# Performance work log

Hardware: AMD Instinct MI355X
Metric: run time of the kernel (lower is better)

## Reference

```python
import jax, jax.numpy as jnp
import numpy as np
import math

HIDDEN = 2048
NUM_HEADS = 16
HEAD_DIM = HIDDEN // NUM_HEADS
B, S = 2, 2048


def setup_inputs() -> dict:
    key = jax.random.key(0)
    k1, k2, k3, k4, k5 = jax.random.split(key, 5)
    scale = 1.0 / math.sqrt(HIDDEN)
    return {
        "hidden_states": jax.random.normal(k1, (B, S, HIDDEN), dtype=jnp.float32),
        "attention_mask": jnp.ones((B, S), dtype=jnp.float32),
        "Wq": jax.random.normal(k2, (HIDDEN, HIDDEN), dtype=jnp.float32) * scale,
        "Wk": jax.random.normal(k3, (HEAD_DIM, HIDDEN), dtype=jnp.float32) * scale,
        "Wv": jax.random.normal(k4, (HEAD_DIM, HIDDEN), dtype=jnp.float32) * scale,
        "Wo": jax.random.normal(k5, (HIDDEN, HIDDEN), dtype=jnp.float32) * scale,
    }


def reference(hidden_states, attention_mask, Wq, Wk, Wv, Wo):
    bsz, tgt, _ = hidden_states.shape
    # projections (torch Linear: x @ W.T)
    q = (hidden_states @ Wq.T).reshape(bsz, tgt, NUM_HEADS, HEAD_DIM).transpose(0, 2, 1, 3)  # [B,H,S,D]
    k = (hidden_states @ Wk.T)[:, None, :, :]  # [B,1,S,D] (MQA single KV head)
    v = (hidden_states @ Wv.T)[:, None, :, :]
    # scores with MQA broadcast (no K expand materialization)
    scores = jnp.einsum("bhsd,bokd->bhsk", q, k) / math.sqrt(HEAD_DIM)  # [B,H,S,S]
    neg = jnp.finfo(scores.dtype).min
    scores = scores + (1.0 - attention_mask)[:, None, None, :] * neg
    probs = jax.nn.softmax(scores, axis=-1)
    attn = jnp.einsum("bhsk,bokd->bhsd", probs, v)  # [B,H,S,D]
    out = attn.transpose(0, 2, 1, 3).reshape(bsz, tgt, HIDDEN) @ Wo.T
    # cache returned by the module (expanded to all heads, as in torch code)
    key_states = jnp.broadcast_to(k, (bsz, NUM_HEADS, tgt, HEAD_DIM))
    value_states = jnp.broadcast_to(v, (bsz, NUM_HEADS, tgt, HEAD_DIM))
    return out, key_states, value_states
```

## Files before the change

### kernel.cpp

```cpp
#include <hip/hip_runtime.h>
#include <hip/hip_bf16.h>
#include <math.h>

#define B_   2
#define S_   2048
#define HID  2048
#define NH   16
#define HD   128

typedef __bf16 bf16_t;
typedef __bf16 bf16x4 __attribute__((ext_vector_type(4)));
typedef __bf16 bf16x8 __attribute__((ext_vector_type(8)));
typedef float  f32x4  __attribute__((ext_vector_type(4)));

__device__ __forceinline__ f32x4 mfma16(bf16x8 a, bf16x8 b, f32x4 c) {
    return __builtin_amdgcn_mfma_f32_16x16x32_bf16(a, b, c, 0, 0, 0);
}

__device__ __forceinline__ void gl2lds16(const void* g, void* l) {
    __builtin_amdgcn_global_load_lds((__attribute__((address_space(1))) void*)(g),
                                     (__attribute__((address_space(3))) void*)(l),
                                     16, 0, 0);
}

__global__ void convert_bf16(const float* __restrict__ s0, const float* __restrict__ s1,
                             const float* __restrict__ s2, const float* __restrict__ s3,
                             const float* __restrict__ s4,
                             bf16_t* __restrict__ d0, bf16_t* __restrict__ d1,
                             bf16_t* __restrict__ d2, bf16_t* __restrict__ d3,
                             bf16_t* __restrict__ d4)
{
    const size_t stride = (size_t)gridDim.x * blockDim.x;
    for (size_t i = (size_t)blockIdx.x * blockDim.x + threadIdx.x; i < 4325376; i += stride) {
        const float* s; bf16_t* d; size_t off;
        if (i < 2097152)      { s = s0; d = d0; off = i; }
        else if (i < 3145728) { s = s1; d = d1; off = i - 2097152; }
        else if (i < 3211264) { s = s2; d = d2; off = i - 3145728; }
        else if (i < 3276800) { s = s3; d = d3; off = i - 3211264; }
        else                  { s = s4; d = d4; off = i - 3276800; }
        float4 v = ((const float4*)s)[off];
        bf16x4 o;
        o[0] = (bf16_t)v.x; o[1] = (bf16_t)v.y; o[2] = (bf16_t)v.z; o[3] = (bf16_t)v.w;
        ((bf16x4*)d)[off] = o;
    }
}

__global__ void broadcast_kv(const bf16_t* __restrict__ k_ws, const bf16_t* __restrict__ v_ws,
                             float* __restrict__ keyo, float* __restrict__ valo)
{
    const size_t stride = (size_t)gridDim.x * blockDim.x;
    for (size_t i = (size_t)blockIdx.x * blockDim.x + threadIdx.x; i < 4194304; i += stride) {
        int which = i >= 2097152;
        size_t f = which ? i - 2097152 : i;
        size_t e = f * 4;
        int d = (int)(e & 127);
        size_t s = (e >> 7) & 2047;
        size_t b = e >> 22;
        const bf16_t* src = (which ? v_ws : k_ws) + (b * S_ + s) * HD + d;
        bf16x4 kv = *(const bf16x4*)src;
        float4 o;
        o.x = (float)kv[0]; o.y = (float)kv[1]; o.z = (float)kv[2]; o.w = (float)kv[3];
        *(float4*)((which ? valo : keyo) + e) = o;
    }
}

template <int MODE>
__global__ __launch_bounds__(256, 2)
void gemm_nt(const bf16_t* __restrict__ A,  const bf16_t* __restrict__ B0,
             const bf16_t* __restrict__ B1, const bf16_t* __restrict__ B2,
             bf16_t* __restrict__ q_ws, bf16_t* __restrict__ k_ws,
             bf16_t* __restrict__ v_ws, bf16_t* __restrict__ vt_ws,
             float* __restrict__ outf)
{
    __shared__ __align__(16) ushort sA[128 * 32];
    __shared__ __align__(16) ushort sB[128 * 32];

    const int tid  = threadIdx.x;
    const int lane = tid & 63;
    const int wave = tid >> 6;
    const int quad = lane >> 4;
    const int l16  = lane & 15;
    const int bn = blockIdx.x, bm = blockIdx.y;
    const int wm = (wave & 1) * 64;
    const int wn = (wave >> 1) * 64;

    const bf16_t* Bbase;
    if (MODE == 0) Bbase = (bn < 16) ? (B0 + (size_t)bn * 128 * HID) : (bn == 16 ? B1 : B2);
    else           Bbase = B0 + (size_t)bn * 128 * HID;
    const bf16_t* Abase = A + (size_t)bm * 128 * HID;

    const int c0 = tid, c1 = tid + 256;
    const int r0 = c0 >> 2, o0 = (c0 & 3) * 8;
    const int r1 = c1 >> 2, o1 = (c1 & 3) * 8;

    f32x4 acc[4][4] = {};

    for (int kt = 0; kt < HID / 32; ++kt) {
        const int ko = kt * 32;
        gl2lds16(Abase + (size_t)r0 * HID + ko + o0, sA + c0 * 8);
        gl2lds16(Abase + (size_t)r1 * HID + ko + o1, sA + c1 * 8);
        gl2lds16(Bbase + (size_t)r0 * HID + ko + o0, sB + c0 * 8);
        gl2lds16(Bbase + (size_t)r1 * HID + ko + o1, sB + c1 * 8);
        __syncthreads();

        bf16x8 af[4], bfr[4];
        for (int mt = 0; mt < 4; ++mt)
            af[mt] = *(const bf16x8*)(sA + (wm + mt * 16 + l16) * 32 + quad * 8);
        for (int nt = 0; nt < 4; ++nt)
            bfr[nt] = *(const bf16x8*)(sB + (wn + nt * 16 + l16) * 32 + quad * 8);
        for (int mt = 0; mt < 4; ++mt)
            for (int nt = 0; nt < 4; ++nt)
                acc[mt][nt] = mfma16(af[mt], bfr[nt], acc[mt][nt]);
        __syncthreads();
    }

    for (int mt = 0; mt < 4; ++mt) {
        for (int nt = 0; nt < 4; ++nt) {
            for (int j = 0; j < 4; ++j) {
                float v = acc[mt][nt][j];
                int row = bm * 128 + wm + mt * 16 + quad * 4 + j;
                int col = wn + nt * 16 + l16;
                if (MODE == 1) {
                    outf[(size_t)row * HID + bn * 128 + col] = v;
                } else {
                    bf16_t bv = (bf16_t)v;
                    if (bn < 16) {
                        q_ws[(size_t)row * HID + bn * 128 + col] = bv;
                    } else {
                        int b = row >> 11, s = row & 2047, d = col;
                        if (bn == 16) {
                            k_ws[((size_t)b * S_ + s) * HD + d] = bv;
                        } else {
                            v_ws[((size_t)b * S_ + s) * HD + d] = bv;
                            vt_ws[((size_t)b * HD + d) * S_ + s] = bv;
                        }
                    }
                }
            }
        }
    }
}

#define SV_U 18432
#define SM_U 27648

__global__ __launch_bounds__(512, 2)
void attn_kernel(const bf16_t* __restrict__ Qw, const bf16_t* __restrict__ Kc,
                 const bf16_t* __restrict__ Vt, const float* __restrict__ mask,
                 bf16_t* __restrict__ Ow)
{
    __shared__ __align__(16) ushort smem[27776];
    float* sMask = (float*)&smem[SM_U];

    const int tid  = threadIdx.x;
    const int lane = tid & 63;
    const int wave = tid >> 6;
    const int quad = lane >> 4;
    const int l16  = lane & 15;
    const int qt = blockIdx.x;
    const int bh = blockIdx.y;
    const int b = bh >> 4, h = bh & 15;

    bf16x8 qf[2][4];
    {
        const bf16_t* qg = Qw + ((size_t)(b * S_ + qt * 256 + wave * 32)) * HID + h * HD;
        for (int mt = 0; mt < 2; ++mt)
            for (int kk = 0; kk < 4; ++kk)
                qf[mt][kk] = *(const bf16x8*)(qg + (size_t)(mt * 16 + l16) * HID + kk * 32 + quad * 8);
    }

    f32x4 oa[2][8] = {};
    float mrow[2][4], lrow[2][4];
    for (int mt = 0; mt < 2; ++mt)
        for (int j = 0; j < 4; ++j) { mrow[mt][j] = -INFINITY; lrow[mt][j] = 0.f; }

    const float scale = 0.08838834764831845f;
    const float NEGF  = -3.4028234663852886e38f;

    const bf16_t* kg = Kc + (size_t)b * S_ * HD;
    const bf16_t* vg = Vt + (size_t)b * HD * S_;

    for (int kt = 0; kt < S_ / 64; ++kt) {
        __syncthreads();
        for (int i = 0; i < 2; ++i) {
            int c = tid + i * 512;
            int kr = c >> 4, kc = (c & 15) * 8;
            *(uint4*)(&smem[kr * 136 + kc]) =
                *(const uint4*)(kg + (size_t)(kt * 64 + kr) * HD + kc);
            int vr = c >> 3, vc = (c & 7) * 8;
            *(uint4*)(&smem[SV_U + vr * 72 + vc]) =
                *(const uint4*)(vg + (size_t)vr * S_ + kt * 64 + vc);
        }
        if (tid < 64) {
            float mv = mask[b * S_ + kt * 64 + tid];
            sMask[tid] = (1.0f - mv) * NEGF;
        }
        __syncthreads();

        f32x4 sa[2][4];
        for (int nt = 0; nt < 4; ++nt) {
            bf16x8 kf[4];
            for (int kk = 0; kk < 4; ++kk)
                kf[kk] = *(const bf16x8*)(&smem[(nt * 16 + l16) * 136 + kk * 32 + quad * 8]);
            for (int mt = 0; mt < 2; ++mt) {
                f32x4 a = {};
                for (int kk = 0; kk < 4; ++kk)
                    a = mfma16(qf[mt][kk], kf[kk], a);
                sa[mt][nt] = a;
            }
        }
        for (int mt = 0; mt < 2; ++mt)
            for (int nt = 0; nt < 4; ++nt) {
                float madd = sMask[nt * 16 + l16];
                for (int j = 0; j < 4; ++j)
                    sa[mt][nt][j] = sa[mt][nt][j] * scale + madd;
            }
        __syncthreads();

        for (int mt = 0; mt < 2; ++mt) {
            float rm[4];
            for (int j = 0; j < 4; ++j) {
                float m = sa[mt][0][j];
                for (int nt = 1; nt < 4; ++nt) m = fmaxf(m, sa[mt][nt][j]);
                rm[j] = m;
            }
            for (int off = 1; off < 16; off <<= 1)
                for (int j = 0; j < 4; ++j)
                    rm[j] = fmaxf(rm[j], __shfl_xor(rm[j], off));
            float alpha[4];
            for (int j = 0; j < 4; ++j) {
                float mnew = fmaxf(mrow[mt][j], rm[j]);
                alpha[j] = __expf(mrow[mt][j] - mnew);
                mrow[mt][j] = mnew;
                lrow[mt][j] *= alpha[j];
                for (int nt = 0; nt < 8; ++nt) oa[mt][nt][j] *= alpha[j];
            }
            float rs[4] = {0.f, 0.f, 0.f, 0.f};
            bf16_t* sPp = (bf16_t*)&smem[wave * 2304];
            for (int nt = 0; nt < 4; ++nt)
                for (int j = 0; j < 4; ++j) {
                    float p = __expf(sa[mt][nt][j] - mrow[mt][j]);
                    rs[j] += p;
                    sPp[(mt * 16 + quad * 4 + j) * 72 + nt * 16 + l16] = (bf16_t)p;
                }
            for (int off = 1; off < 16; off <<= 1)
                for (int j = 0; j < 4; ++j) rs[j] += __shfl_xor(rs[j], off);
            for (int j = 0; j < 4; ++j) lrow[mt][j] += rs[j];
        }

        bf16x8 pf[2][2];
        for (int mt = 0; mt < 2; ++mt)
            for (int kk = 0; kk < 2; ++kk)
                pf[mt][kk] = *(const bf16x8*)(&smem[wave * 2304 + (mt * 16 + l16) * 72 + kk * 32 + quad * 8]);
        for (int nt = 0; nt < 8; ++nt)
            for (int kk = 0; kk < 2; ++kk) {
                bf16x8 vf = *(const bf16x8*)(&smem[SV_U + (nt * 16 + l16) * 72 + kk * 32 + quad * 8]);
                for (int mt = 0; mt < 2; ++mt)
                    oa[mt][nt] = mfma16(pf[mt][kk], vf, oa[mt][nt]);
            }
    }

    for (int mt = 0; mt < 2; ++mt)
        for (int j = 0; j < 4; ++j) {
            float inv = 1.0f / lrow[mt][j];
            int s = qt * 256 + wave * 32 + mt * 16 + quad * 4 + j;
            for (int nt = 0; nt < 8; ++nt) {
                int d = nt * 16 + l16;
                Ow[((size_t)(b * S_ + s)) * HID + h * HD + d] = (bf16_t)(oa[mt][nt][j] * inv);
            }
        }
}

extern "C" void kernel_launch(void* const* d_in, const int* in_sizes, int n_in,
                              void* d_out, int out_size, void* d_ws, size_t ws_size,
                              hipStream_t stream) {
    const float* hs   = (const float*)d_in[0];
    const float* mask = (const float*)d_in[1];
    const float* Wq   = (const float*)d_in[2];
    const float* Wk   = (const float*)d_in[3];
    const float* Wv   = (const float*)d_in[4];
    const float* Wo   = (const float*)d_in[5];
    float* out = (float*)d_out;

    bf16_t* wqb = (bf16_t*)out;
    bf16_t* wkb = wqb + 4194304;
    bf16_t* wvb = wkb + 262144;
    bf16_t* qb  = (bf16_t*)(out + 8388608);
    bf16_t* wob = (bf16_t*)(out + 12582912);
    bf16_t* hsb = (bf16_t*)(out + 16777216);
    bf16_t* o_ws = hsb;

    bf16_t* k_ws  = (bf16_t*)d_ws;
    bf16_t* v_ws  = k_ws + 524288;
    bf16_t* vt_ws = v_ws + 524288;

    convert_bf16<<<2048, 256, 0, stream>>>(hs, Wq, Wk, Wv, Wo, hsb, wqb, wkb, wvb, wob);
    gemm_nt<0><<<dim3(18, 32), 256, 0, stream>>>(hsb, wqb, wkb, wvb, qb, k_ws, v_ws, vt_ws, nullptr);
    attn_kernel<<<dim3(8, 32), 512, 0, stream>>>(qb, k_ws, vt_ws, mask, o_ws);
    gemm_nt<1><<<dim3(16, 32), 256, 0, stream>>>(o_ws, wob, nullptr, nullptr, nullptr, nullptr, nullptr, nullptr, out);
    broadcast_kv<<<4096, 256, 0, stream>>>(k_ws, v_ws, out + 8388608, out + 16777216);
}
```

Before: 407.7 us.

## Shrink attention query tile to 16 rows per wave, add lazy rescale and exp2

The attention kernel now has each wave own 16 query rows instead of 32, so a block covers 128 rows. The grid doubles to 512 blocks, and shared memory and registers shrink so launch bounds can ask for 4 blocks per CU, which should fill the 256-CU part better. It also folds log2e into the scale to use exp2f, and skips the online-softmax rescale unless a row max grows by more than 8. The cost is half the Q reuse per K/V tile load, so each tile is reloaded by twice as many blocks.

New measurement: 421.7 us. 1.03x slower.

```diff
diff --git a/kernel.cpp b/kernel.cpp
--- a/kernel.cpp
+++ b/kernel.cpp
@@ -141,15 +141,15 @@
     }
 }
 
-#define SV_U 18432
-#define SM_U 27648
-
-__global__ __launch_bounds__(512, 2)
+#define SV_U 9216
+#define SM_U 18432
+
+__global__ __launch_bounds__(512, 4)
 void attn_kernel(const bf16_t* __restrict__ Qw, const bf16_t* __restrict__ Kc,
                  const bf16_t* __restrict__ Vt, const float* __restrict__ mask,
                  bf16_t* __restrict__ Ow)
 {
-    __shared__ __align__(16) ushort smem[27776];
+    __shared__ __align__(16) ushort smem[18560];
     float* sMask = (float*)&smem[SM_U];
 
     const int tid  = threadIdx.x;
@@ -161,21 +161,20 @@
     const int bh = blockIdx.y;
     const int b = bh >> 4, h = bh & 15;
 
-    bf16x8 qf[2][4];
+    bf16x8 qf[4];
     {
-        const bf16_t* qg = Qw + ((size_t)(b * S_ + qt * 256 + wave * 32)) * HID + h * HD;
-        for (int mt = 0; mt < 2; ++mt)
-            for (int kk = 0; kk < 4; ++kk)
-                qf[mt][kk] = *(const bf16x8*)(qg + (size_t)(mt * 16 + l16) * HID + kk * 32 + quad * 8);
-    }
-
-    f32x4 oa[2][8] = {};
-    float mrow[2][4], lrow[2][4];
-    for (int mt = 0; mt < 2; ++mt)
-        for (int j = 0; j < 4; ++j) { mrow[mt][j] = -INFINITY; lrow[mt][j] = 0.f; }
-
-    const float scale = 0.08838834764831845f;
-    const float NEGF  = -3.4028234663852886e38f;
+        const bf16_t* qg = Qw + ((size_t)(b * S_ + qt * 128 + wave * 16 + l16)) * HID + h * HD;
+        for (int kk = 0; kk < 4; ++kk)
+            qf[kk] = *(const bf16x8*)(qg + kk * 32 + quad * 8);
+    }
+
+    f32x4 oa[8] = {};
+    float mrow[4], lrow[4];
+    for (int j = 0; j < 4; ++j) { mrow[j] = -INFINITY; lrow[j] = 0.f; }
+
+    const float scale2 = 0.08838834764831845f * 1.4426950408889634f;
+    const float NEGF   = -3.4028234663852886e38f;
+    const float LOG2E  = 1.4426950408889634f;
 
     const bf16_t* kg = Kc + (size_t)b * S_ * HD;
     const bf16_t* vg = Vt + (size_t)b * HD * S_;
@@ -192,83 +191,74 @@
                 *(const uint4*)(vg + (size_t)vr * S_ + kt * 64 + vc);
         }
         if (tid < 64) {
-            float mv = mask[b * S_ + kt * 64 + tid];
-            sMask[tid] = (1.0f - mv) * NEGF;
-        }
-        __syncthreads();
-
-        f32x4 sa[2][4];
+            float t = (1.0f - mask[b * S_ + kt * 64 + tid]) * NEGF;
+            sMask[tid] = t * LOG2E;
+        }
+        __syncthreads();
+
+        f32x4 sa[4] = {};
+        for (int kk = 0; kk < 4; ++kk)
+            for (int nt = 0; nt < 4; ++nt) {
+                bf16x8 kf = *(const bf16x8*)(&smem[(nt * 16 + l16) * 136 + kk * 32 + quad * 8]);
+                sa[nt] = mfma16(qf[kk], kf, sa[nt]);
+            }
         for (int nt = 0; nt < 4; ++nt) {
-            bf16x8 kf[4];
-            for (int kk = 0; kk < 4; ++kk)
-                kf[kk] = *(const bf16x8*)(&smem[(nt * 16 + l16) * 136 + kk * 32 + quad * 8]);
-            for (int mt = 0; mt < 2; ++mt) {
-                f32x4 a = {};
-                for (int kk = 0; kk < 4; ++kk)
-                    a = mfma16(qf[mt][kk], kf[kk], a);
-                sa[mt][nt] = a;
-            }
-        }
-        for (int mt = 0; mt < 2; ++mt)
-            for (int nt = 0; nt < 4; ++nt) {
-                float madd = sMask[nt * 16 + l16];
-                for (int j = 0; j < 4; ++j)
-                    sa[mt][nt][j] = sa[mt][nt][j] * scale + madd;
-            }
-        __syncthreads();
-
-        for (int mt = 0; mt < 2; ++mt) {
-            float rm[4];
+            float madd = sMask[nt * 16 + l16];
+            for (int j = 0; j < 4; ++j)
+                sa[nt][j] = sa[nt][j] * scale2 + madd;
+        }
+        __syncthreads();
+
+        float rm[4];
+        for (int j = 0; j < 4; ++j) {
+            float m = sa[0][j];
+            for (int nt = 1; nt < 4; ++nt) m = fmaxf(m, sa[nt][j]);
+            rm[j] = m;
+        }
+        for (int off = 1; off < 16; off <<= 1)
+            for (int j = 0; j < 4; ++j)
+                rm[j] = fmaxf(rm[j], __shfl_xor(rm[j], off));
+        bool need = false;
+        for (int j = 0; j < 4; ++j) need = need || (rm[j] > mrow[j] + 8.0f);
+        if (__any((int)need)) {
             for (int j = 0; j < 4; ++j) {
-                float m = sa[mt][0][j];
-                for (int nt = 1; nt < 4; ++nt) m = fmaxf(m, sa[mt][nt][j]);
-                rm[j] = m;
-            }
-            for (int off = 1; off < 16; off <<= 1)
-                for (int j = 0; j < 4; ++j)
-                    rm[j] = fmaxf(rm[j], __shfl_xor(rm[j], off));
-            float alpha[4];
+                float mnew  = fmaxf(mrow[j], rm[j]);
+                float alpha = exp2f(mrow[j] - mnew);
+                mrow[j] = mnew;
+                lrow[j] *= alpha;
+                for (int nt = 0; nt < 8; ++nt) oa[nt][j] *= alpha;
+            }
+        }
+        float rs[4] = {0.f, 0.f, 0.f, 0.f};
+        bf16_t* sPp = (bf16_t*)&smem[wave * 1152];
+        for (int nt = 0; nt < 4; ++nt)
             for (int j = 0; j < 4; ++j) {
-                float mnew = fmaxf(mrow[mt][j], rm[j]);
-                alpha[j] = __expf(mrow[mt][j] - mnew);
-                mrow[mt][j] = mnew;
-                lrow[mt][j] *= alpha[j];
-                for (int nt = 0; nt < 8; ++nt) oa[mt][nt][j] *= alpha[j];
-            }
-            float rs[4] = {0.f, 0.f, 0.f, 0.f};
-            bf16_t* sPp = (bf16_t*)&smem[wave * 2304];
-            for (int nt = 0; nt < 4; ++nt)
-                for (int j = 0; j < 4; ++j) {
-                    float p = __expf(sa[mt][nt][j] - mrow[mt][j]);
-                    rs[j] += p;
-                    sPp[(mt * 16 + quad * 4 + j) * 72 + nt * 16 + l16] = (bf16_t)p;
-                }
-            for (int off = 1; off < 16; off <<= 1)
-                for (int j = 0; j < 4; ++j) rs[j] += __shfl_xor(rs[j], off);
-            for (int j = 0; j < 4; ++j) lrow[mt][j] += rs[j];
-        }
-
-        bf16x8 pf[2][2];
-        for (int mt = 0; mt < 2; ++mt)
-            for (int kk = 0; kk < 2; ++kk)
-                pf[mt][kk] = *(const bf16x8*)(&smem[wave * 2304 + (mt * 16 + l16) * 72 + kk * 32 + quad * 8]);
-        for (int nt = 0; nt < 8; ++nt)
-            for (int kk = 0; kk < 2; ++kk) {
+                float p = exp2f(sa[nt][j] - mrow[j]);
+                rs[j] += p;
+                sPp[(quad * 4 + j) * 72 + nt * 16 + l16] = (bf16_t)p;
+            }
+        for (int off = 1; off < 16; off <<= 1)
+            for (int j = 0; j < 4; ++j) rs[j] += __shfl_xor(rs[j], off);
+        for (int j = 0; j < 4; ++j) lrow[j] += rs[j];
+
+        bf16x8 pf[2];
+        for (int kk = 0; kk < 2; ++kk)
+            pf[kk] = *(const bf16x8*)(&smem[wave * 1152 + l16 * 72 + kk * 32 + quad * 8]);
+        for (int kk = 0; kk < 2; ++kk)
+            for (int nt = 0; nt < 8; ++nt) {
                 bf16x8 vf = *(const bf16x8*)(&smem[SV_U + (nt * 16 + l16) * 72 + kk * 32 + quad * 8]);
-                for (int mt = 0; mt < 2; ++mt)
-                    oa[mt][nt] = mfma16(pf[mt][kk], vf, oa[mt][nt]);
-            }
-    }
-
-    for (int mt = 0; mt < 2; ++mt)
-        for (int j = 0; j < 4; ++j) {
-            float inv = 1.0f / lrow[mt][j];
-            int s = qt * 256 + wave * 32 + mt * 16 + quad * 4 + j;
-            for (int nt = 0; nt < 8; ++nt) {
-                int d = nt * 16 + l16;
-                Ow[((size_t)(b * S_ + s)) * HID + h * HD + d] = (bf16_t)(oa[mt][nt][j] * inv);
-            }
-        }
+                oa[nt] = mfma16(pf[kk], vf, oa[nt]);
+            }
+    }
+
+    for (int j = 0; j < 4; ++j) {
+        float inv = 1.0f / lrow[j];
+        int s = qt * 128 + wave * 16 + quad * 4 + j;
+        for (int nt = 0; nt < 8; ++nt) {
+            int d = nt * 16 + l16;
+            Ow[((size_t)(b * S_ + s)) * HID + h * HD + d] = (bf16_t)(oa[nt][j] * inv);
+        }
+    }
 }
 
 extern "C" void kernel_launch(void* const* d_in, const int* in_sizes, int n_in,
@@ -296,7 +286,7 @@
 
     convert_bf16<<<2048, 256, 0, stream>>>(hs, Wq, Wk, Wv, Wo, hsb, wqb, wkb, wvb, wob);
     gemm_nt<0><<<dim3(18, 32), 256, 0, stream>>>(hsb, wqb, wkb, wvb, qb, k_ws, v_ws, vt_ws, nullptr);
-    attn_kernel<<<dim3(8, 32), 512, 0, stream>>>(qb, k_ws, vt_ws, mask, o_ws);
+    attn_kernel<<<dim3(16, 32), 512, 0, stream>>>(qb, k_ws, vt_ws, mask, o_ws);
     gemm_nt<1><<<dim3(16, 32), 256, 0, stream>>>(o_ws, wob, nullptr, nullptr, nullptr, nullptr, nullptr, nullptr, out);
     broadcast_kv<<<4096, 256, 0, stream>>>(k_ws, v_ws, out + 8388608, out + 16777216);
 }
```

## Prefetch K/V tiles into registers, shrink attention blocks, use exp2 with lazy rescale

Applied to the files above, without the earlier changes.

The attention kernel now loads the next K/V tile and mask slice into registers while the current tile is being computed, then writes them to LDS at the top of the next iteration. This hides global-load latency behind the MFMA and softmax work. Blocks shrink from 512 to 256 threads, with 128 queries each, and the grid doubles to 512 blocks so more blocks fit per CU. Softmax folds log2e into the scale and uses exp2f, and it skips the output rescale unless some row max has grown by more than a threshold. The cost is more registers per thread and a more involved online-softmax path.

New measurement: 485.7 us. 1.19x slower.

```diff
diff --git a/kernel.cpp b/kernel.cpp
--- a/kernel.cpp
+++ b/kernel.cpp
@@ -141,15 +141,15 @@
     }
 }
 
-#define SV_U 18432
-#define SM_U 27648
-
-__global__ __launch_bounds__(512, 2)
+#define SV_U 9216
+#define SM_U 18432
+
+__global__ __launch_bounds__(256, 2)
 void attn_kernel(const bf16_t* __restrict__ Qw, const bf16_t* __restrict__ Kc,
                  const bf16_t* __restrict__ Vt, const float* __restrict__ mask,
                  bf16_t* __restrict__ Ow)
 {
-    __shared__ __align__(16) ushort smem[27776];
+    __shared__ __align__(16) ushort smem[18560];
     float* sMask = (float*)&smem[SM_U];
 
     const int tid  = threadIdx.x;
@@ -161,109 +161,166 @@
     const int bh = blockIdx.y;
     const int b = bh >> 4, h = bh & 15;
 
+    int koff[4], voff[4], klds[4], vlds[4];
+#pragma unroll
+    for (int i = 0; i < 4; ++i) {
+        int c = tid + i * 256;
+        koff[i] = (c >> 4) * HD + (c & 15) * 8;
+        klds[i] = (c >> 4) * 136 + (c & 15) * 8;
+        voff[i] = (c >> 3) * S_ + (c & 7) * 8;
+        vlds[i] = SV_U + (c >> 3) * 72 + (c & 7) * 8;
+    }
+
+    const bf16_t* kg = Kc + (size_t)b * S_ * HD;
+    const bf16_t* vg = Vt + (size_t)b * HD * S_;
+
     bf16x8 qf[2][4];
     {
-        const bf16_t* qg = Qw + ((size_t)(b * S_ + qt * 256 + wave * 32)) * HID + h * HD;
+        const bf16_t* qg = Qw + ((size_t)(b * S_ + qt * 128 + wave * 32)) * HID + h * HD;
+#pragma unroll
         for (int mt = 0; mt < 2; ++mt)
+#pragma unroll
             for (int kk = 0; kk < 4; ++kk)
                 qf[mt][kk] = *(const bf16x8*)(qg + (size_t)(mt * 16 + l16) * HID + kk * 32 + quad * 8);
     }
 
     f32x4 oa[2][8] = {};
     float mrow[2][4], lrow[2][4];
+#pragma unroll
     for (int mt = 0; mt < 2; ++mt)
+#pragma unroll
         for (int j = 0; j < 4; ++j) { mrow[mt][j] = -INFINITY; lrow[mt][j] = 0.f; }
 
-    const float scale = 0.08838834764831845f;
-    const float NEGF  = -3.4028234663852886e38f;
-
-    const bf16_t* kg = Kc + (size_t)b * S_ * HD;
-    const bf16_t* vg = Vt + (size_t)b * HD * S_;
+    const float scale2 = 0.08838834764831845f * 1.4426950408889634f;
+    const float NEGF   = -3.4028234663852886e38f;
+    const float LOG2E  = 1.4426950408889634f;
+
+    uint4 kreg[4], vreg[4];
+    float mreg = 1.0f;
+#pragma unroll
+    for (int i = 0; i < 4; ++i) {
+        kreg[i] = *(const uint4*)(kg + koff[i]);
+        vreg[i] = *(const uint4*)(vg + voff[i]);
+    }
+    if (tid < 64) mreg = mask[b * S_ + tid];
 
     for (int kt = 0; kt < S_ / 64; ++kt) {
         __syncthreads();
-        for (int i = 0; i < 2; ++i) {
-            int c = tid + i * 512;
-            int kr = c >> 4, kc = (c & 15) * 8;
-            *(uint4*)(&smem[kr * 136 + kc]) =
-                *(const uint4*)(kg + (size_t)(kt * 64 + kr) * HD + kc);
-            int vr = c >> 3, vc = (c & 7) * 8;
-            *(uint4*)(&smem[SV_U + vr * 72 + vc]) =
-                *(const uint4*)(vg + (size_t)vr * S_ + kt * 64 + vc);
-        }
-        if (tid < 64) {
-            float mv = mask[b * S_ + kt * 64 + tid];
-            sMask[tid] = (1.0f - mv) * NEGF;
-        }
-        __syncthreads();
-
-        f32x4 sa[2][4];
+#pragma unroll
+        for (int i = 0; i < 4; ++i) {
+            *(uint4*)(&smem[klds[i]]) = kreg[i];
+            *(uint4*)(&smem[vlds[i]]) = vreg[i];
+        }
+        if (tid < 64) sMask[tid] = (1.0f - mreg) * NEGF * LOG2E;
+        __syncthreads();
+
+        f32x4 sa[2][4] = {};
+#pragma unroll
+        for (int kk = 0; kk < 4; ++kk)
+#pragma unroll
+            for (int nt = 0; nt < 4; ++nt) {
+                bf16x8 kf = *(const bf16x8*)(&smem[(nt * 16 + l16) * 136 + kk * 32 + quad * 8]);
+#pragma unroll
+                for (int mt = 0; mt < 2; ++mt)
+                    sa[mt][nt] = mfma16(qf[mt][kk], kf, sa[mt][nt]);
+            }
+#pragma unroll
         for (int nt = 0; nt < 4; ++nt) {
-            bf16x8 kf[4];
-            for (int kk = 0; kk < 4; ++kk)
-                kf[kk] = *(const bf16x8*)(&smem[(nt * 16 + l16) * 136 + kk * 32 + quad * 8]);
-            for (int mt = 0; mt < 2; ++mt) {
-                f32x4 a = {};
-                for (int kk = 0; kk < 4; ++kk)
-                    a = mfma16(qf[mt][kk], kf[kk], a);
-                sa[mt][nt] = a;
-            }
-        }
+            float madd = sMask[nt * 16 + l16];
+#pragma unroll
+            for (int mt = 0; mt < 2; ++mt)
+#pragma unroll
+                for (int j = 0; j < 4; ++j)
+                    sa[mt][nt][j] = sa[mt][nt][j] * scale2 + madd;
+        }
+        __syncthreads();
+
+        float rm[2][4];
+#pragma unroll
         for (int mt = 0; mt < 2; ++mt)
-            for (int nt = 0; nt < 4; ++nt) {
-                float madd = sMask[nt * 16 + l16];
-                for (int j = 0; j < 4; ++j)
-                    sa[mt][nt][j] = sa[mt][nt][j] * scale + madd;
-            }
-        __syncthreads();
-
-        for (int mt = 0; mt < 2; ++mt) {
-            float rm[4];
+#pragma unroll
             for (int j = 0; j < 4; ++j) {
                 float m = sa[mt][0][j];
                 for (int nt = 1; nt < 4; ++nt) m = fmaxf(m, sa[mt][nt][j]);
-                rm[j] = m;
-            }
-            for (int off = 1; off < 16; off <<= 1)
+                rm[mt][j] = m;
+            }
+        for (int off = 1; off < 16; off <<= 1)
+#pragma unroll
+            for (int mt = 0; mt < 2; ++mt)
+#pragma unroll
                 for (int j = 0; j < 4; ++j)
-                    rm[j] = fmaxf(rm[j], __shfl_xor(rm[j], off));
-            float alpha[4];
-            for (int j = 0; j < 4; ++j) {
-                float mnew = fmaxf(mrow[mt][j], rm[j]);
-                alpha[j] = __expf(mrow[mt][j] - mnew);
-                mrow[mt][j] = mnew;
-                lrow[mt][j] *= alpha[j];
-                for (int nt = 0; nt < 8; ++nt) oa[mt][nt][j] *= alpha[j];
-            }
+                    rm[mt][j] = fmaxf(rm[mt][j], __shfl_xor(rm[mt][j], off));
+        bool need = false;
+#pragma unroll
+        for (int mt = 0; mt < 2; ++mt)
+#pragma unroll
+            for (int j = 0; j < 4; ++j)
+                need = need || (rm[mt][j] > mrow[mt][j] + 8.0f);
+        if (__any((int)need)) {
+#pragma unroll
+            for (int mt = 0; mt < 2; ++mt)
+#pragma unroll
+                for (int j = 0; j < 4; ++j) {
+                    float mnew  = fmaxf(mrow[mt][j], rm[mt][j]);
+                    float alpha = exp2f(mrow[mt][j] - mnew);
+                    mrow[mt][j] = mnew;
+                    lrow[mt][j] *= alpha;
+                    for (int nt = 0; nt < 8; ++nt) oa[mt][nt][j] *= alpha;
+                }
+        }
+        bf16_t* sPp = (bf16_t*)&smem[wave * 2304];
+#pragma unroll
+        for (int mt = 0; mt < 2; ++mt) {
             float rs[4] = {0.f, 0.f, 0.f, 0.f};
-            bf16_t* sPp = (bf16_t*)&smem[wave * 2304];
+#pragma unroll
             for (int nt = 0; nt < 4; ++nt)
+#pragma unroll
                 for (int j = 0; j < 4; ++j) {
-                    float p = __expf(sa[mt][nt][j] - mrow[mt][j]);
+                    float p = exp2f(sa[mt][nt][j] - mrow[mt][j]);
                     rs[j] += p;
                     sPp[(mt * 16 + quad * 4 + j) * 72 + nt * 16 + l16] = (bf16_t)p;
                 }
             for (int off = 1; off < 16; off <<= 1)
+#pragma unroll
                 for (int j = 0; j < 4; ++j) rs[j] += __shfl_xor(rs[j], off);
+#pragma unroll
             for (int j = 0; j < 4; ++j) lrow[mt][j] += rs[j];
         }
 
+        if (kt + 1 < S_ / 64) {
+            const bf16_t* kgn = kg + (size_t)(kt + 1) * 64 * HD;
+            const bf16_t* vgn = vg + (kt + 1) * 64;
+#pragma unroll
+            for (int i = 0; i < 4; ++i) {
+                kreg[i] = *(const uint4*)(kgn + koff[i]);
+                vreg[i] = *(const uint4*)(vgn + voff[i]);
+            }
+            if (tid < 64) mreg = mask[b * S_ + (kt + 1) * 64 + tid];
+        }
+
         bf16x8 pf[2][2];
+#pragma unroll
         for (int mt = 0; mt < 2; ++mt)
+#pragma unroll
             for (int kk = 0; kk < 2; ++kk)
                 pf[mt][kk] = *(const bf16x8*)(&smem[wave * 2304 + (mt * 16 + l16) * 72 + kk * 32 + quad * 8]);
-        for (int nt = 0; nt < 8; ++nt)
-            for (int kk = 0; kk < 2; ++kk) {
+#pragma unroll
+        for (int kk = 0; kk < 2; ++kk)
+#pragma unroll
+            for (int nt = 0; nt < 8; ++nt) {
                 bf16x8 vf = *(const bf16x8*)(&smem[SV_U + (nt * 16 + l16) * 72 + kk * 32 + quad * 8]);
+#pragma unroll
                 for (int mt = 0; mt < 2; ++mt)
                     oa[mt][nt] = mfma16(pf[mt][kk], vf, oa[mt][nt]);
             }
     }
 
+#pragma unroll
     for (int mt = 0; mt < 2; ++mt)
+#pragma unroll
         for (int j = 0; j < 4; ++j) {
             float inv = 1.0f / lrow[mt][j];
-            int s = qt * 256 + wave * 32 + mt * 16 + quad * 4 + j;
+            int s = qt * 128 + wave * 32 + mt * 16 + quad * 4 + j;
             for (int nt = 0; nt < 8; ++nt) {
                 int d = nt * 16 + l16;
                 Ow[((size_t)(b * S_ + s)) * HID + h * HD + d] = (bf16_t)(oa[mt][nt][j] * inv);
@@ -296,7 +353,7 @@
 
     convert_bf16<<<2048, 256, 0, stream>>>(hs, Wq, Wk, Wv, Wo, hsb, wqb, wkb, wvb, wob);
     gemm_nt<0><<<dim3(18, 32), 256, 0, stream>>>(hsb, wqb, wkb, wvb, qb, k_ws, v_ws, vt_ws, nullptr);
-    attn_kernel<<<dim3(8, 32), 512, 0, stream>>>(qb, k_ws, vt_ws, mask, o_ws);
+    attn_kernel<<<dim3(16, 32), 256, 0, stream>>>(qb, k_ws, vt_ws, mask, o_ws);
     gemm_nt<1><<<dim3(16, 32), 256, 0, stream>>>(o_ws, wob, nullptr, nullptr, nullptr, nullptr, nullptr, nullptr, out);
     broadcast_kv<<<4096, 256, 0, stream>>>(k_ws, v_ws, out + 8388608, out + 16777216);
 }
```
